# Kernel tuning notes

Hardware: AMD Instinct MI355X
Metric: run time of the kernel (lower is better)

## Reference

```python
import math
import jax, jax.numpy as jnp
import numpy as np

B, T, D, H = 4, 1024, 1024, 8
HD = D // H  # head_dim = 128

def _trigram_dirs():
    # 8 trigrams = all sign combinations in {−1,+1}^3, L2-normalized (p=2, dim=1)
    t = np.array([[(i >> b & 1) * 2 - 1 for b in (2, 1, 0)] for i in range(8)], dtype=np.float32)
    return jnp.asarray(t / np.linalg.norm(t, axis=1, keepdims=True))

def setup_inputs() -> dict:
    key = jax.random.key(0)
    k1, k2, k3, k4 = jax.random.split(key, 4)
    x = jax.random.normal(k1, (B, T, D), dtype=jnp.float32)
    Wqkv = jax.random.normal(k2, (D, 3 * D), dtype=jnp.float32) * 0.02
    Wout = jax.random.normal(k3, (D, D), dtype=jnp.float32) * 0.02
    # head_scales init to 0 in the module; use nonzero values so the geo-bias path is exercised
    head_scales = jax.random.normal(k4, (H,), dtype=jnp.float32) * 0.1
    head_dirs = _trigram_dirs()  # [H, 3] buffer
    return {"x": x, "Wqkv": Wqkv, "Wout": Wout, "head_scales": head_scales, "head_dirs": head_dirs}

def reference(x, Wqkv, Wout, head_scales, head_dirs):
    b, t, d = x.shape
    scale = 1.0 / math.sqrt(HD)
    qkv = (x @ Wqkv).reshape(b, t, 3, H, HD)
    qkv = jnp.transpose(qkv, (2, 0, 3, 1, 4))  # [3, B, H, T, HD]
    q, k, v = qkv[0], qkv[1], qkv[2]
    # scores: [B, H, T, T]
    scores = jnp.einsum('bhqd,bhkd->bhqk', q, k) * scale
    # rank-1 trigram geometric bias from first 3 dims of q/k
    q_proj = jnp.einsum('bhtd,hd->bht', q[..., :3], head_dirs)
    k_proj = jnp.einsum('bhtd,hd->bht', k[..., :3], head_dirs)
    geo_bias = q_proj[..., :, None] * k_proj[..., None, :]  # [B, H, T, T]
    scores = scores + head_scales[None, :, None, None] * geo_bias
    causal = jnp.tril(jnp.ones((t, t), dtype=bool))
    scores = jnp.where(causal, scores, -jnp.inf)
    attn = jax.nn.softmax(scores, axis=-1)
    out = jnp.einsum('bhqk,bhkd->bhqd', attn, v)  # [B, H, T, HD]
    out = jnp.transpose(out, (0, 2, 1, 3)).reshape(b, t, d)
    return out @ Wout
```

## Files before the change

kernel.cpp:

```cpp
#include <hip/hip_runtime.h>
#include <stdint.h>

typedef __attribute__((ext_vector_type(8))) short short8;
typedef __attribute__((ext_vector_type(4))) short short4v;
typedef __attribute__((ext_vector_type(4))) float f32x4;

__device__ __forceinline__ short f2bf(float x) {
  union { float f; uint32_t u; } c; c.f = x;
  uint32_t r = (c.u + 0x7FFFu + ((c.u >> 16) & 1u)) >> 16;
  return (short)r;
}
__device__ __forceinline__ float b2f(short s) {
  union { uint32_t u; float f; } c; c.u = ((uint32_t)(uint16_t)s) << 16;
  return c.f;
}
__device__ __forceinline__ uint32_t pack2bf(float lo, float hi) {
  return ((uint32_t)(uint16_t)f2bf(hi) << 16) | (uint32_t)(uint16_t)f2bf(lo);
}

__global__ __launch_bounds__(256) void cvt_kernel(const float* __restrict__ in,
                                                  short* __restrict__ out, int n4) {
  int i = blockIdx.x * 256 + threadIdx.x;
  const int stride = gridDim.x * 256;
  for (; i < n4; i += stride) {
    float4 v = reinterpret_cast<const float4*>(in)[i];
    short4v o;
    o.x = f2bf(v.x); o.y = f2bf(v.y); o.z = f2bf(v.z); o.w = f2bf(v.w);
    reinterpret_cast<short4v*>(out)[i] = o;
  }
}

__global__ __launch_bounds__(256) void tcvt_kernel(const float* __restrict__ in,
                                                   short* __restrict__ out, int K, int N) {
  __shared__ __align__(16) short tile[32][33];
  const int nb = blockIdx.x * 32, kb = blockIdx.y * 32;
  const int tx = threadIdx.x & 31, ty = threadIdx.x >> 5;
#pragma unroll
  for (int i = 0; i < 32; i += 8)
    tile[ty + i][tx] = f2bf(in[(size_t)(kb + ty + i) * N + nb + tx]);
  __syncthreads();
#pragma unroll
  for (int i = 0; i < 32; i += 8)
    out[(size_t)(nb + ty + i) * K + kb + tx] = tile[tx][ty + i];
}

__global__ __launch_bounds__(256) void vtrans_kernel(const short* __restrict__ qkvb,
                                                     short* __restrict__ vT) {
  __shared__ __align__(16) short tile[64][65];
  const int b = blockIdx.z;
  const int kv0 = blockIdx.x * 64, c0 = blockIdx.y * 64;
  const int tx = threadIdx.x & 15, ty = threadIdx.x >> 4;
  const short* src = qkvb + (size_t)(b * 1024) * 3072 + 2048;
#pragma unroll
  for (int i = 0; i < 64; i += 16) {
    int r = ty + i;
#pragma unroll
    for (int j = 0; j < 4; ++j)
      tile[r][tx * 4 + j] = src[(size_t)(kv0 + r) * 3072 + c0 + tx * 4 + j];
  }
  __syncthreads();
  short* dst = vT + (size_t)b * 1024 * 1024;
#pragma unroll
  for (int i = 0; i < 64; i += 16) {
    int cc = ty + i;
#pragma unroll
    for (int j = 0; j < 4; ++j)
      dst[(size_t)(c0 + cc) * 1024 + kv0 + tx * 4 + j] = tile[tx * 4 + j][cc];
  }
}

__global__ __launch_bounds__(256) void kproj_kernel(const short* __restrict__ qkvb,
                                                    const float* __restrict__ hdirs,
                                                    float* __restrict__ kproj) {
  const int i = blockIdx.x * 256 + threadIdx.x;
  const int bh = i >> 10, tt = i & 1023;
  const int b = bh >> 3, h = bh & 7;
  const float d0 = hdirs[h * 3], d1 = hdirs[h * 3 + 1], d2 = hdirs[h * 3 + 2];
  const short* kr = qkvb + (size_t)(b * 1024 + tt) * 3072 + 1024 + h * 128;
  kproj[i] = b2f(kr[0]) * d0 + b2f(kr[1]) * d1 + b2f(kr[2]) * d2;
}

template <int OUT_BF16>
__global__ __launch_bounds__(256) void gemm_kernel(const short* __restrict__ A,
                                                   const short* __restrict__ Bt,
                                                   void* __restrict__ Cout,
                                                   int K, int ldc) {
  __shared__ __align__(16) short Al[2][128 * 32];
  __shared__ __align__(16) short Bl[2][128 * 32];
  const int t = threadIdx.x;
  const int lane = t & 63, w = t >> 6;
  const int wr = w >> 1, wc = w & 1;
  const int g = lane >> 4, c16 = lane & 15;
  const int row0 = blockIdx.y * 128, col0 = blockIdx.x * 128;

  f32x4 acc[4][4];
#pragma unroll
  for (int m = 0; m < 4; ++m)
#pragma unroll
    for (int n = 0; n < 4; ++n) {
      f32x4 z = {0.0f, 0.0f, 0.0f, 0.0f};
      acc[m][n] = z;
    }

  auto stage = [&](int buf, int kt) {
    const int k0 = kt * 32;
#pragma unroll
    for (int i = 0; i < 2; ++i) {
      const int qb = i * 256 + (t & 192);
      const int q = qb + lane;
      const int r = q >> 2;
      const int c = (q & 3) ^ ((r >> 1) & 3);
      const short* ga = A + (size_t)(row0 + r) * K + k0 + c * 8;
      const short* gb = Bt + (size_t)(col0 + r) * K + k0 + c * 8;
      __builtin_amdgcn_global_load_lds((const __attribute__((address_space(1))) void*)ga,
                                       (__attribute__((address_space(3))) void*)&Al[buf][qb * 8],
                                       16, 0, 0);
      __builtin_amdgcn_global_load_lds((const __attribute__((address_space(1))) void*)gb,
                                       (__attribute__((address_space(3))) void*)&Bl[buf][qb * 8],
                                       16, 0, 0);
    }
  };

  stage(0, 0);
  __syncthreads();
  const int NK = K >> 5;
  int cur = 0;
  const int rA0 = wr * 64 + c16;
  const int rB0 = wc * 64 + c16;
  for (int kt = 0; kt < NK; ++kt) {
    if (kt + 1 < NK) stage(cur ^ 1, kt + 1);
    short8 aF[4], bF[4];
#pragma unroll
    for (int m = 0; m < 4; ++m) {
      const int r = rA0 + m * 16;
      const int c = g ^ ((r >> 1) & 3);
      aF[m] = *reinterpret_cast<const short8*>(&Al[cur][r * 32 + c * 8]);
    }
#pragma unroll
    for (int n = 0; n < 4; ++n) {
      const int r = rB0 + n * 16;
      const int c = g ^ ((r >> 1) & 3);
      bF[n] = *reinterpret_cast<const short8*>(&Bl[cur][r * 32 + c * 8]);
    }
#pragma unroll
    for (int m = 0; m < 4; ++m)
#pragma unroll
      for (int n = 0; n < 4; ++n)
        acc[m][n] = __builtin_amdgcn_mfma_f32_16x16x32_bf16(aF[m], bF[n], acc[m][n], 0, 0, 0);
    __syncthreads();
    cur ^= 1;
  }

  const int er = row0 + wr * 64 + g * 4;
  const int ec = col0 + wc * 64 + c16;
#pragma unroll
  for (int m = 0; m < 4; ++m)
#pragma unroll
    for (int n = 0; n < 4; ++n)
#pragma unroll
      for (int j = 0; j < 4; ++j) {
        const size_t off = (size_t)(er + m * 16 + j) * ldc + ec + n * 16;
        if (OUT_BF16)
          ((short*)Cout)[off] = f2bf(acc[m][n][j]);
        else
          ((float*)Cout)[off] = acc[m][n][j];
      }
}

__global__ __launch_bounds__(256) void attn_kernel(const short* __restrict__ qkvb,
                                                   const short* __restrict__ vT,
                                                   const float* __restrict__ head_scales,
                                                   const float* __restrict__ hdirs,
                                                   const float* __restrict__ kproj,
                                                   short* __restrict__ attnb) {
  __shared__ __align__(16) short Kl[2][64 * 128];
  __shared__ __align__(16) short Vl[2][128 * 64];
  __shared__ float kp_lds[2][64];

  const int bid = blockIdx.x;
  const int bh = (bid & 7) * 4 + ((bid >> 3) & 3);
  const int r2 = bid >> 5;
  const int qt = (bid < 256) ? (15 - r2) : (r2 - 8);
  const int b = bh >> 3, h = bh & 7;
  const int t = threadIdx.x, lane = t & 63, w = t >> 6;
  const int g = lane >> 4, c16 = lane & 15;
  const int q0w = qt * 64 + w * 16;
  const int q_abs = q0w + c16;

  const short* qbase = qkvb + (size_t)(b * 1024) * 3072 + h * 128;
  const short* kbase = qbase + 1024;
  const short* vtb = vT + (size_t)bh * 128 * 1024;
  const float* kp = kproj + bh * 1024;

  const float LOG2E = 1.44269504088896f;
  const float scale2 = 0.08838834764831845f * 1.44269504088896f;

  short8 aQ[4];
  float hqp;
  {
    const short* qr = qbase + (size_t)(q0w + c16) * 3072;
#pragma unroll
    for (int kk = 0; kk < 4; ++kk)
      aQ[kk] = *reinterpret_cast<const short8*>(qr + kk * 32 + g * 8);
    const float hs = head_scales[h];
    hqp = hs * LOG2E *
          (b2f(qr[0]) * hdirs[h * 3] + b2f(qr[1]) * hdirs[h * 3 + 1] + b2f(qr[2]) * hdirs[h * 3 + 2]);
  }

  float m_s = -1e30f, l_s = 0.0f;
  f32x4 accO[8];
#pragma unroll
  for (int d = 0; d < 8; ++d) {
    f32x4 z = {0.0f, 0.0f, 0.0f, 0.0f};
    accO[d] = z;
  }

  auto stageKV = [&](int buf, int kvt) {
    const int kv0 = kvt * 64;
#pragma unroll
    for (int i = 0; i < 4; ++i) {
      const int s = w * 4 + i;
      {
        const int r = s * 4 + g;
        const int c = c16 ^ (r & 7);
        const short* ga = kbase + (size_t)(kv0 + r) * 3072 + c * 8;
        __builtin_amdgcn_global_load_lds((const __attribute__((address_space(1))) void*)ga,
                                         (__attribute__((address_space(3))) void*)&Kl[buf][s * 512],
                                         16, 0, 0);
      }
      {
        const int r = s * 8 + (lane >> 3);
        const int c = (lane & 7) ^ (r & 7);
        const short* ga = vtb + (size_t)r * 1024 + kv0 + c * 8;
        __builtin_amdgcn_global_load_lds((const __attribute__((address_space(1))) void*)ga,
                                         (__attribute__((address_space(3))) void*)&Vl[buf][s * 512],
                                         16, 0, 0);
      }
    }
    if (lane < 16) kp_lds[buf][w * 16 + lane] = kp[kv0 + w * 16 + lane];
  };

  const int nkv = qt + 1;
  stageKV(0, 0);
  __syncthreads();
  int cur = 0;
  for (int kvt = 0; kvt < nkv; ++kvt) {
    const int kv0 = kvt * 64;
    if (kvt + 1 < nkv) stageKV(cur ^ 1, kvt + 1);
    const short* Kc = Kl[cur];
    const short* Vc = Vl[cur];
    const float* kpc = kp_lds[cur];

    float p[4][4];
#pragma unroll
    for (int n = 0; n < 4; ++n) {
      f32x4 s4 = {0.0f, 0.0f, 0.0f, 0.0f};
      const int r = n * 16 + c16;
#pragma unroll
      for (int kk = 0; kk < 4; ++kk) {
        const int cch = (kk * 4 + g) ^ (r & 7);
        short8 bK = *reinterpret_cast<const short8*>(&Kc[r * 128 + cch * 8]);
        s4 = __builtin_amdgcn_mfma_f32_16x16x32_bf16(bK, aQ[kk], s4, 0, 0, 0);
      }
#pragma unroll
      for (int j = 0; j < 4; ++j) {
        const int kloc = n * 16 + g * 4 + j;
        const float v = s4[j] * scale2 + hqp * kpc[kloc];
        p[n][j] = (kv0 + kloc <= q_abs) ? v : -1e30f;
      }
    }

    float mx;
    {
      float a0 = fmaxf(fmaxf(p[0][0], p[0][1]), fmaxf(p[0][2], p[0][3]));
      float a1 = fmaxf(fmaxf(p[1][0], p[1][1]), fmaxf(p[1][2], p[1][3]));
      float a2 = fmaxf(fmaxf(p[2][0], p[2][1]), fmaxf(p[2][2], p[2][3]));
      float a3 = fmaxf(fmaxf(p[3][0], p[3][1]), fmaxf(p[3][2], p[3][3]));
      mx = fmaxf(fmaxf(a0, a1), fmaxf(a2, a3));
      mx = fmaxf(mx, __shfl_xor(mx, 16, 64));
      mx = fmaxf(mx, __shfl_xor(mx, 32, 64));
    }

    if (__any(mx - m_s > 11.54f)) {
      const float mn = fmaxf(m_s, mx);
      const float alpha = exp2f(m_s - mn);
      m_s = mn;
      l_s *= alpha;
      float aO[4];
#pragma unroll
      for (int j = 0; j < 4; ++j) aO[j] = __shfl(alpha, g * 4 + j, 64);
#pragma unroll
      for (int d = 0; d < 8; ++d)
#pragma unroll
        for (int j = 0; j < 4; ++j) accO[d][j] *= aO[j];
    }

    float s01 = 0.0f, s23 = 0.0f;
#pragma unroll
    for (int n = 0; n < 4; ++n) {
      float e0 = exp2f(p[n][0] - m_s), e1 = exp2f(p[n][1] - m_s);
      float e2 = exp2f(p[n][2] - m_s), e3 = exp2f(p[n][3] - m_s);
      p[n][0] = e0; p[n][1] = e1; p[n][2] = e2; p[n][3] = e3;
      if (n < 2) s01 += (e0 + e1) + (e2 + e3); else s23 += (e0 + e1) + (e2 + e3);
    }
    float sum = s01 + s23;
    sum += __shfl_xor(sum, 16, 64);
    sum += __shfl_xor(sum, 32, 64);
    l_s += sum;

    uint32_t pk[4][2];
#pragma unroll
    for (int n = 0; n < 4; ++n) {
      pk[n][0] = pack2bf(p[n][0], p[n][1]);
      pk[n][1] = pack2bf(p[n][2], p[n][3]);
    }

    union { uint32_t d[4]; short8 s; } aPu[2];
#pragma unroll
    for (int kk = 0; kk < 2; ++kk)
#pragma unroll
      for (int wd = 0; wd < 4; ++wd) {
        const int src = (2 * (g & 1) + (wd >> 1)) * 16 + c16;
        const uint32_t v0 = (uint32_t)__shfl((int)pk[kk * 2][wd & 1], src, 64);
        const uint32_t v1 = (uint32_t)__shfl((int)pk[kk * 2 + 1][wd & 1], src, 64);
        aPu[kk].d[wd] = (g >= 2) ? v1 : v0;
      }

#pragma unroll
    for (int dt = 0; dt < 8; ++dt) {
      const int r = dt * 16 + c16;
#pragma unroll
      for (int kk = 0; kk < 2; ++kk) {
        const int cch = (kk * 4 + g) ^ (r & 7);
        short8 bV = *reinterpret_cast<const short8*>(&Vc[r * 64 + cch * 8]);
        accO[dt] = __builtin_amdgcn_mfma_f32_16x16x32_bf16(aPu[kk].s, bV, accO[dt], 0, 0, 0);
      }
    }
    __syncthreads();
    cur ^= 1;
  }

  float linv[4];
#pragma unroll
  for (int j = 0; j < 4; ++j) linv[j] = 1.0f / __shfl(l_s, g * 4 + j, 64);
#pragma unroll
  for (int j = 0; j < 4; ++j) {
    const size_t rowoff = (size_t)(b * 1024 + q0w + g * 4 + j) * 1024 + h * 128;
#pragma unroll
    for (int dt = 0; dt < 8; ++dt)
      attnb[rowoff + dt * 16 + c16] = f2bf(accO[dt][j] * linv[j]);
  }
}

extern "C" void kernel_launch(void* const* d_in, const int* in_sizes, int n_in,
                              void* d_out, int out_size, void* d_ws, size_t ws_size,
                              hipStream_t stream) {
  const float* x = (const float*)d_in[0];
  const float* Wqkv = (const float*)d_in[1];
  const float* Wout = (const float*)d_in[2];
  const float* hscale = (const float*)d_in[3];
  const float* hdirs = (const float*)d_in[4];
  float* out = (float*)d_out;

  char* ws = (char*)d_ws;
  short* xb = (short*)(ws);
  short* wqkvT = (short*)(ws + (size_t)8 * 1024 * 1024);
  short* woutT = (short*)(ws + (size_t)14 * 1024 * 1024);
  short* qkvb = (short*)(ws + (size_t)16 * 1024 * 1024);
  short* vT = (short*)(ws + (size_t)40 * 1024 * 1024);
  short* attnb = (short*)(ws + (size_t)48 * 1024 * 1024);
  float* kproj = (float*)(ws);

  cvt_kernel<<<2048, 256, 0, stream>>>(x, xb, (4 * 1024 * 1024) / 4);
  tcvt_kernel<<<dim3(96, 32), 256, 0, stream>>>(Wqkv, wqkvT, 1024, 3072);
  tcvt_kernel<<<dim3(32, 32), 256, 0, stream>>>(Wout, woutT, 1024, 1024);
  gemm_kernel<1><<<dim3(24, 32), 256, 0, stream>>>(xb, wqkvT, (void*)qkvb, 1024, 3072);
  kproj_kernel<<<128, 256, 0, stream>>>(qkvb, hdirs, kproj);
  vtrans_kernel<<<dim3(16, 16, 4), 256, 0, stream>>>(qkvb, vT);
  attn_kernel<<<512, 256, 0, stream>>>(qkvb, vT, hscale, hdirs, kproj, attnb);
  gemm_kernel<0><<<dim3(8, 32), 256, 0, stream>>>(attnb, woutT, out, 1024, 1024);
}
```

Before: 118.7 us.

## Read V directly from global memory instead of staging through LDS

Removes the double-buffered V tile from shared memory and has each wave load its V fragments straight from global (transposed V) right before the PV MFMAs. The launch-bounds hint also now requests 4 blocks per CU, since LDS use is halved and occupancy can rise. The trade-off is that V loads are no longer prefetched asynchronously, so global latency sits on the critical path and each of the four waves re-reads the same V data through L1/L2.

```diff
diff --git a/kernel.cpp b/kernel.cpp
--- a/kernel.cpp
+++ b/kernel.cpp
@@ -167,14 +167,13 @@
       }
 }
 
-__global__ __launch_bounds__(256) void attn_kernel(const short* __restrict__ qkvb,
-                                                   const short* __restrict__ vT,
-                                                   const float* __restrict__ head_scales,
-                                                   const float* __restrict__ hdirs,
-                                                   const float* __restrict__ kproj,
-                                                   short* __restrict__ attnb) {
+__global__ __launch_bounds__(256, 4) void attn_kernel(const short* __restrict__ qkvb,
+                                                      const short* __restrict__ vT,
+                                                      const float* __restrict__ head_scales,
+                                                      const float* __restrict__ hdirs,
+                                                      const float* __restrict__ kproj,
+                                                      short* __restrict__ attnb) {
   __shared__ __align__(16) short Kl[2][64 * 128];
-  __shared__ __align__(16) short Vl[2][128 * 64];
   __shared__ float kp_lds[2][64];
 
   const int bid = blockIdx.x;
@@ -215,40 +214,29 @@
     accO[d] = z;
   }
 
-  auto stageKV = [&](int buf, int kvt) {
+  auto stageK = [&](int buf, int kvt) {
     const int kv0 = kvt * 64;
 #pragma unroll
     for (int i = 0; i < 4; ++i) {
       const int s = w * 4 + i;
-      {
-        const int r = s * 4 + g;
-        const int c = c16 ^ (r & 7);
-        const short* ga = kbase + (size_t)(kv0 + r) * 3072 + c * 8;
-        __builtin_amdgcn_global_load_lds((const __attribute__((address_space(1))) void*)ga,
-                                         (__attribute__((address_space(3))) void*)&Kl[buf][s * 512],
-                                         16, 0, 0);
-      }
-      {
-        const int r = s * 8 + (lane >> 3);
-        const int c = (lane & 7) ^ (r & 7);
-        const short* ga = vtb + (size_t)r * 1024 + kv0 + c * 8;
-        __builtin_amdgcn_global_load_lds((const __attribute__((address_space(1))) void*)ga,
-                                         (__attribute__((address_space(3))) void*)&Vl[buf][s * 512],
-                                         16, 0, 0);
-      }
+      const int r = s * 4 + g;
+      const int c = c16 ^ (r & 7);
+      const short* ga = kbase + (size_t)(kv0 + r) * 3072 + c * 8;
+      __builtin_amdgcn_global_load_lds((const __attribute__((address_space(1))) void*)ga,
+                                       (__attribute__((address_space(3))) void*)&Kl[buf][s * 512],
+                                       16, 0, 0);
     }
     if (lane < 16) kp_lds[buf][w * 16 + lane] = kp[kv0 + w * 16 + lane];
   };
 
   const int nkv = qt + 1;
-  stageKV(0, 0);
+  stageK(0, 0);
   __syncthreads();
   int cur = 0;
   for (int kvt = 0; kvt < nkv; ++kvt) {
     const int kv0 = kvt * 64;
-    if (kvt + 1 < nkv) stageKV(cur ^ 1, kvt + 1);
+    if (kvt + 1 < nkv) stageK(cur ^ 1, kvt + 1);
     const short* Kc = Kl[cur];
-    const short* Vc = Vl[cur];
     const float* kpc = kp_lds[cur];
 
     float p[4][4];
@@ -328,13 +316,11 @@
 
 #pragma unroll
     for (int dt = 0; dt < 8; ++dt) {
-      const int r = dt * 16 + c16;
-#pragma unroll
-      for (int kk = 0; kk < 2; ++kk) {
-        const int cch = (kk * 4 + g) ^ (r & 7);
-        short8 bV = *reinterpret_cast<const short8*>(&Vc[r * 64 + cch * 8]);
-        accO[dt] = __builtin_amdgcn_mfma_f32_16x16x32_bf16(aPu[kk].s, bV, accO[dt], 0, 0, 0);
-      }
+      const short* vrow = vtb + (size_t)(dt * 16 + c16) * 1024 + kv0 + g * 8;
+      short8 bV0 = *reinterpret_cast<const short8*>(vrow);
+      short8 bV1 = *reinterpret_cast<const short8*>(vrow + 32);
+      accO[dt] = __builtin_amdgcn_mfma_f32_16x16x32_bf16(aPu[0].s, bV0, accO[dt], 0, 0, 0);
+      accO[dt] = __builtin_amdgcn_mfma_f32_16x16x32_bf16(aPu[1].s, bV1, accO[dt], 0, 0, 0);
     }
     __syncthreads();
     cur ^= 1;
```

Measured after the change: 157.7 us. 32.8% more time.
